# Performance work log

Measured on AMD Instinct MI355X. Metric: run time of the kernel, lower is better.

The kernel has to match this reference:

```python
import jax, jax.numpy as jnp
import numpy as np

N_SAMPLES = 8388608  # total packed samples across all rays
N_RAYS = 131072      # number of rays (segments)


def setup_inputs() -> dict:
    key = jax.random.key(0)
    k1, k2, k3 = jax.random.split(key, 3)
    # Sorted segment ids emulate the packed ray layout (samples of a ray are contiguous).
    segment_ids = jnp.sort(
        jax.random.randint(k1, (N_SAMPLES,), 0, N_RAYS, dtype=jnp.int32)
    )
    rgb_samples = jax.random.normal(k2, (N_SAMPLES, 3), dtype=jnp.float32)
    weights_samples = jax.random.uniform(k3, (N_SAMPLES, 1), dtype=jnp.float32)
    return {
        "segment_ids": segment_ids,
        "rgb_samples": rgb_samples,
        "weights_samples": weights_samples,
        "n_rays": N_RAYS,
    }


def reference(segment_ids, rgb_samples, weights_samples, n_rays):
    # pred_rgb[r] = sum over samples s belonging to ray r of w_s * rgb_s
    weighted = rgb_samples * weights_samples  # [N,3], weight broadcast over channels
    pred_rgb = jax.ops.segment_sum(weighted, segment_ids, num_segments=n_rays)  # [n_rays,3]
    return pred_rgb
```

## Files before the change

### kernel.cpp

```cpp
#include <hip/hip_runtime.h>


#define NTHREADS 256
#define WAVES_PER_BLOCK (NTHREADS / 64)
#define CPL 4
#define CHUNK (64 * CPL)
#define CHUNKS 8
#define SPW (CHUNK * CHUNKS)

__global__ __launch_bounds__(NTHREADS) void zero_out_kernel(float4* __restrict__ out4,
                                                            int n4) {
  int i = blockIdx.x * blockDim.x + threadIdx.x;
  if (i < n4) out4[i] = make_float4(0.f, 0.f, 0.f, 0.f);
}

__device__ __forceinline__ void process_chunk(const int4 id4, const float4 w4,
                                              const float4 r0, const float4 r1,
                                              const float4 r2, const int lane,
                                              float* __restrict__ out) {
  int idv[CPL] = {id4.x, id4.y, id4.z, id4.w};
  float px[CPL], py[CPL], pz[CPL];
  px[0] = r0.x * w4.x; py[0] = r0.y * w4.x; pz[0] = r0.z * w4.x;
  px[1] = r0.w * w4.y; py[1] = r1.x * w4.y; pz[1] = r1.y * w4.y;
  px[2] = r1.z * w4.z; py[2] = r1.w * w4.z; pz[2] = r2.x * w4.z;
  px[3] = r2.y * w4.w; py[3] = r2.z * w4.w; pz[3] = r2.w * w4.w;

  const int first_id = idv[0];
  int run_id = first_id;
  float rx = px[0], ry = py[0], rz = pz[0];
  float hx = 0.f, hy = 0.f, hz = 0.f;
  bool f_intra = false;
  #pragma unroll
  for (int k = 1; k < CPL; ++k) {
    if (idv[k] == run_id) {
      rx += px[k]; ry += py[k]; rz += pz[k];
    } else {
      if (!f_intra) {
        hx = rx; hy = ry; hz = rz; f_intra = true;
      } else {
        atomicAdd(&out[3 * run_id + 0], rx);
        atomicAdd(&out[3 * run_id + 1], ry);
        atomicAdd(&out[3 * run_id + 2], rz);
      }
      run_id = idv[k];
      rx = px[k]; ry = py[k]; rz = pz[k];
    }
  }
  const int last_id = run_id;

  const int prev_tid = __shfl_up(last_id, 1, 64);
  int fl = (lane == 0 || f_intra || prev_tid != first_id) ? 1 : 0;
  float sx = rx, sy = ry, sz = rz;
  #pragma unroll
  for (int off = 1; off < 64; off <<= 1) {
    const float ox = __shfl_up(sx, off, 64);
    const float oy = __shfl_up(sy, off, 64);
    const float oz = __shfl_up(sz, off, 64);
    const int ofl = __shfl_up(fl, off, 64);
    if (lane >= off && fl == 0) { sx += ox; sy += oy; sz += oz; fl = ofl; }
  }

  const float pSx = __shfl_up(sx, 1, 64);
  const float pSy = __shfl_up(sy, 1, 64);
  const float pSz = __shfl_up(sz, 1, 64);
  if (f_intra) {
    const bool link = (lane > 0) && (prev_tid == first_id);
    atomicAdd(&out[3 * first_id + 0], hx + (link ? pSx : 0.f));
    atomicAdd(&out[3 * first_id + 1], hy + (link ? pSy : 0.f));
    atomicAdd(&out[3 * first_id + 2], hz + (link ? pSz : 0.f));
  }

  const int next_hid = __shfl_down(first_id, 1, 64);
  if (lane == 63 || next_hid != last_id) {
    atomicAdd(&out[3 * last_id + 0], sx);
    atomicAdd(&out[3 * last_id + 1], sy);
    atomicAdd(&out[3 * last_id + 2], sz);
  }
}

__global__ __launch_bounds__(NTHREADS, 4) void integrate_kernel(
    const int* __restrict__ ids, const float* __restrict__ rgb,
    const float* __restrict__ w, float* __restrict__ out, int n_samples) {
  const int lane = threadIdx.x & 63;
  const long long wave_id =
      (long long)blockIdx.x * WAVES_PER_BLOCK + (threadIdx.x >> 6);
  const long long span0 = wave_id * SPW;
  if (span0 >= (long long)n_samples) return;

  if (span0 + SPW <= (long long)n_samples) {
    const long long lb = span0 + (long long)lane * CPL;
    int4 Ai; float4 Aw, Ar0, Ar1, Ar2;
    int4 Bi; float4 Bw, Br0, Br1, Br2;
#define LOADX(P, c)                                   \
    do {                                              \
      const long long b_ = lb + (long long)(c) * CHUNK; \
      P##i  = *(const int4*)(ids + b_);               \
      P##w  = *(const float4*)(w + b_);               \
      P##r0 = *(const float4*)(rgb + 3 * b_);         \
      P##r1 = *(const float4*)(rgb + 3 * b_ + 4);     \
      P##r2 = *(const float4*)(rgb + 3 * b_ + 8);     \
    } while (0)
    LOADX(A, 0);
    #pragma unroll
    for (int c = 0; c < CHUNKS; c += 2) {
      LOADX(B, c + 1);
      process_chunk(Ai, Aw, Ar0, Ar1, Ar2, lane, out);
      if (c + 2 < CHUNKS) LOADX(A, c + 2);
      process_chunk(Bi, Bw, Br0, Br1, Br2, lane, out);
    }
#undef LOADX
  } else {
    const int last = ids[n_samples - 1];
    for (int c = 0; c < CHUNKS; ++c) {
      const long long cb = span0 + (long long)c * CHUNK;
      if (cb >= (long long)n_samples) break;
      int idt[CPL]; float wt[CPL], rt[3 * CPL];
      #pragma unroll
      for (int j = 0; j < CPL; ++j) {
        const long long s = cb + (long long)lane * CPL + j;
        if (s < (long long)n_samples) {
          idt[j] = ids[s];
          wt[j] = w[s];
          rt[3 * j + 0] = rgb[3 * s + 0];
          rt[3 * j + 1] = rgb[3 * s + 1];
          rt[3 * j + 2] = rgb[3 * s + 2];
        } else {
          idt[j] = (j == 0) ? last : idt[j - 1];
          wt[j] = 0.f;
          rt[3 * j + 0] = rt[3 * j + 1] = rt[3 * j + 2] = 0.f;
        }
      }
      const int4 i4 = make_int4(idt[0], idt[1], idt[2], idt[3]);
      const float4 w4 = make_float4(wt[0], wt[1], wt[2], wt[3]);
      const float4 r0 = make_float4(rt[0], rt[1], rt[2], rt[3]);
      const float4 r1 = make_float4(rt[4], rt[5], rt[6], rt[7]);
      const float4 r2 = make_float4(rt[8], rt[9], rt[10], rt[11]);
      process_chunk(i4, w4, r0, r1, r2, lane, out);
    }
  }
}

extern "C" void kernel_launch(void* const* d_in, const int* in_sizes, int n_in,
                              void* d_out, int out_size, void* d_ws, size_t ws_size,
                              hipStream_t stream) {
  const int*   segment_ids = (const int*)d_in[0];
  const float* rgb         = (const float*)d_in[1];
  const float* weights     = (const float*)d_in[2];
  float*       out         = (float*)d_out;

  const int n_samples = in_sizes[0];

  {
    int n4 = out_size / 4;
    int blocks = (n4 + NTHREADS - 1) / NTHREADS;
    zero_out_kernel<<<blocks, NTHREADS, 0, stream>>>((float4*)out, n4);
  }
  {
    long long waves = ((long long)n_samples + SPW - 1) / SPW;
    int blocks = (int)((waves + WAVES_PER_BLOCK - 1) / WAVES_PER_BLOCK);
    integrate_kernel<<<blocks, NTHREADS, 0, stream>>>(
        segment_ids, rgb, weights, out, n_samples);
  }
}
```

Baseline: 201.8 us.

## Stage chunk loads through LDS with async global_load_lds double buffering

Replaces the register double-buffered global loads with direct global-to-LDS asynchronous loads into a per-wave double buffer, using explicit vmcnt waits to overlap the next chunk's fetch with processing of the current one. Lanes then read their strided rgb triples from LDS. The occupancy hint in launch bounds is dropped. It adds LDS traffic, possible bank conflicts on the 48-byte stride reads, and relies on hand-written waitcnt counts being correct, since the atomics in process_chunk also affect vmcnt.

```diff
diff --git a/kernel.cpp b/kernel.cpp
--- a/kernel.cpp
+++ b/kernel.cpp
@@ -7,11 +7,21 @@
 #define CHUNK (64 * CPL)
 #define CHUNKS 8
 #define SPW (CHUNK * CHUNKS)
+#define CHUNK_BYTES (CHUNK * 20)
+#define IDS_OFF 0
+#define W_OFF 1024
+#define RGB_OFF 2048
 
 __global__ __launch_bounds__(NTHREADS) void zero_out_kernel(float4* __restrict__ out4,
                                                             int n4) {
   int i = blockIdx.x * blockDim.x + threadIdx.x;
   if (i < n4) out4[i] = make_float4(0.f, 0.f, 0.f, 0.f);
+}
+
+__device__ __forceinline__ void gll16(const void* g, void* l) {
+  __builtin_amdgcn_global_load_lds(
+      (const __attribute__((address_space(1))) void*)g,
+      (__attribute__((address_space(3))) void*)l, 16, 0, 0);
 }
 
 __device__ __forceinline__ void process_chunk(const int4 id4, const float4 w4,
@@ -78,37 +88,56 @@
   }
 }
 
-__global__ __launch_bounds__(NTHREADS, 4) void integrate_kernel(
+__global__ __launch_bounds__(NTHREADS) void integrate_kernel(
     const int* __restrict__ ids, const float* __restrict__ rgb,
     const float* __restrict__ w, float* __restrict__ out, int n_samples) {
+  __shared__ char lds[WAVES_PER_BLOCK * 2 * CHUNK_BYTES];
   const int lane = threadIdx.x & 63;
-  const long long wave_id =
-      (long long)blockIdx.x * WAVES_PER_BLOCK + (threadIdx.x >> 6);
+  const int wib = threadIdx.x >> 6;
+  char* mybuf = lds + wib * (2 * CHUNK_BYTES);
+
+  const long long wave_id = (long long)blockIdx.x * WAVES_PER_BLOCK + wib;
   const long long span0 = wave_id * SPW;
   if (span0 >= (long long)n_samples) return;
 
   if (span0 + SPW <= (long long)n_samples) {
-    const long long lb = span0 + (long long)lane * CPL;
-    int4 Ai; float4 Aw, Ar0, Ar1, Ar2;
-    int4 Bi; float4 Bw, Br0, Br1, Br2;
-#define LOADX(P, c)                                   \
-    do {                                              \
-      const long long b_ = lb + (long long)(c) * CHUNK; \
-      P##i  = *(const int4*)(ids + b_);               \
-      P##w  = *(const float4*)(w + b_);               \
-      P##r0 = *(const float4*)(rgb + 3 * b_);         \
-      P##r1 = *(const float4*)(rgb + 3 * b_ + 4);     \
-      P##r2 = *(const float4*)(rgb + 3 * b_ + 8);     \
+    const char* gid = (const char*)(ids + span0) + lane * 16;
+    const char* gw  = (const char*)(w + span0) + lane * 16;
+    const char* grg = (const char*)(rgb + 3 * span0) + lane * 16;
+
+#define STAGE(c, b)                                                     \
+    do {                                                                \
+      const long long o_ = (long long)(c) * (CHUNK * 4);                \
+      char* lb_ = mybuf + (b) * CHUNK_BYTES;                            \
+      gll16(gid + o_, lb_ + IDS_OFF);                                   \
+      gll16(gw + o_, lb_ + W_OFF);                                      \
+      gll16(grg + 3 * o_, lb_ + RGB_OFF);                               \
+      gll16(grg + 3 * o_ + 1024, lb_ + RGB_OFF + 1024);                 \
+      gll16(grg + 3 * o_ + 2048, lb_ + RGB_OFF + 2048);                 \
     } while (0)
-    LOADX(A, 0);
+
+    STAGE(0, 0);
+    STAGE(1, 1);
     #pragma unroll
-    for (int c = 0; c < CHUNKS; c += 2) {
-      LOADX(B, c + 1);
-      process_chunk(Ai, Aw, Ar0, Ar1, Ar2, lane, out);
-      if (c + 2 < CHUNKS) LOADX(A, c + 2);
-      process_chunk(Bi, Bw, Br0, Br1, Br2, lane, out);
+    for (int c = 0; c < CHUNKS; ++c) {
+      if (c < CHUNKS - 1) {
+        asm volatile("s_waitcnt vmcnt(5)" ::: "memory");
+      } else {
+        asm volatile("s_waitcnt vmcnt(0)" ::: "memory");
+      }
+      const char* lb = mybuf + (c & 1) * CHUNK_BYTES;
+      const int4   i4 = *(const int4*)(lb + IDS_OFF + lane * 16);
+      const float4 w4 = *(const float4*)(lb + W_OFF + lane * 16);
+      const float4 r0 = *(const float4*)(lb + RGB_OFF + lane * 48);
+      const float4 r1 = *(const float4*)(lb + RGB_OFF + lane * 48 + 16);
+      const float4 r2 = *(const float4*)(lb + RGB_OFF + lane * 48 + 32);
+      process_chunk(i4, w4, r0, r1, r2, lane, out);
+      if (c + 2 < CHUNKS) {
+        asm volatile("s_waitcnt lgkmcnt(0)" ::: "memory");
+        STAGE(c + 2, c & 1);
+      }
     }
-#undef LOADX
+#undef STAGE
   } else {
     const int last = ids[n_samples - 1];
     for (int c = 0; c < CHUNKS; ++c) {
```

New measurement: 202.2 us. About the same (+0.2%).
